# Optimization experiments

Measured on AMD Instinct MI355X. Metric: run time of the kernel, lower is better.

The kernel has to match this reference:

```python
import jax, jax.numpy as jnp
import numpy as np

B, N1, N2, C = 4, 1024, 128, 1152
H, D = 16, 72            # num_heads, head_dim (1152 = 16*72)
HID = 4608               # mlp hidden = 4*1152
ATTN_SCALE = D ** -0.5
RMS_SCALE = C ** 0.5     # quirk: RMSNorm built with dim=1152 though applied over d=72
LN_EPS = 1e-6


def setup_inputs() -> dict:
    key = jax.random.key(0)
    ks = iter(jax.random.split(key, 64))
    n = lambda shape, s=1.0: jax.random.normal(next(ks), shape, jnp.float32) * s
    W = 0.02  # weight init scale
    inp = {
        "x": n((B, N1, C)),
        "c": n((B, N2, C)),
        "global_c": n((B, C)),
        "ada_x_w": n((C, 6 * C), W), "ada_x_b": jnp.zeros((6 * C,)),
        "ada_c_w": n((C, 6 * C), W), "ada_c_b": jnp.zeros((6 * C,)),
        "g1x_g": jnp.ones((C,)), "g1x_b": jnp.zeros((C,)),
        "g2x_g": jnp.ones((C,)), "g2x_b": jnp.zeros((C,)),
        "g1c_g": jnp.ones((C,)), "g1c_b": jnp.zeros((C,)),
        "g2c_g": jnp.ones((C,)), "g2c_b": jnp.zeros((C,)),
        "qkv_x_w": n((C, 3 * C), W), "qkv_x_b": jnp.zeros((3 * C,)),
        "proj_x_w": n((C, C), W), "proj_x_b": jnp.zeros((C,)),
        "qkv_c_w": n((C, 3 * C), W), "qkv_c_b": jnp.zeros((3 * C,)),
        "proj_c_w": n((C, C), W), "proj_c_b": jnp.zeros((C,)),
        "gq_x": jnp.ones((1,)), "gk_x": jnp.ones((1,)),
        "gq_c": jnp.ones((1,)), "gk_c": jnp.ones((1,)),
        "mlp_x_w1": n((C, HID), W), "mlp_x_b1": jnp.zeros((HID,)),
        "mlp_x_w2": n((HID, C), W), "mlp_x_b2": jnp.zeros((C,)),
        "mlp_c_w1": n((C, HID), W), "mlp_c_b1": jnp.zeros((HID,)),
        "mlp_c_w2": n((HID, C), W), "mlp_c_b2": jnp.zeros((C,)),
    }
    return inp


def _ln(t, g, b):
    m = t.mean(-1, keepdims=True)
    v = ((t - m) ** 2).mean(-1, keepdims=True)
    return (t - m) * jax.lax.rsqrt(v + LN_EPS) * g + b


def _modulate(t, shift, scale):  # shift/scale: [B, C]
    return t * (1.0 + scale[:, None, :]) + shift[:, None, :]


def _rms(t, g):  # F.normalize over last dim, then * sqrt(1152) * g
    nrm = jnp.sqrt(jnp.sum(t * t, axis=-1, keepdims=True))
    return t / jnp.maximum(nrm, 1e-12) * (RMS_SCALE * g)


def _heads(t):  # [B, N, H*D] -> [B, H, N, D]
    Bq, Nq, _ = t.shape
    return t.reshape(Bq, Nq, H, D).transpose(0, 2, 1, 3)


def _mmdit_forward(x, c, global_c,
                   ada_x_w, ada_x_b, ada_c_w, ada_c_b,
                   g1x_g, g1x_b, g2x_g, g2x_b, g1c_g, g1c_b, g2c_g, g2c_b,
                   qkv_x_w, qkv_x_b, proj_x_w, proj_x_b,
                   qkv_c_w, qkv_c_b, proj_c_w, proj_c_b,
                   gq_x, gk_x, gq_c, gk_c,
                   mlp_x_w1, mlp_x_b1, mlp_x_w2, mlp_x_b2,
                   mlp_c_w1, mlp_c_b1, mlp_c_w2, mlp_c_b2):
    s = jax.nn.silu(global_c)
    mod_x = jnp.split(s @ ada_x_w + ada_x_b, 6, axis=-1)
    mod_c = jnp.split(s @ ada_c_w + ada_c_b, 6, axis=-1)
    (sh_msa_x, sc_msa_x, gt_msa_x, sh_mlp_x, sc_mlp_x, gt_mlp_x) = mod_x
    (sh_msa_c, sc_msa_c, gt_msa_c, sh_mlp_c, sc_mlp_c, gt_mlp_c) = mod_c

    xin = _modulate(_ln(x, g1x_g, g1x_b), sh_msa_x, sc_msa_x)
    cin = _modulate(_ln(c, g1c_g, g1c_b), sh_msa_c, sc_msa_c)

    qx, kx, vx = jnp.split(xin @ qkv_x_w + qkv_x_b, 3, axis=-1)
    qc, kc, vc = jnp.split(cin @ qkv_c_w + qkv_c_b, 3, axis=-1)
    qx, kx, vx = _heads(qx), _heads(kx), _heads(vx)
    qc, kc, vc = _heads(qc), _heads(kc), _heads(vc)
    qx, kx = _rms(qx, gq_x), _rms(kx, gk_x)
    qc, kc = _rms(qc, gq_c), _rms(kc, gk_c)

    q = jnp.concatenate([qx, qc], axis=2)  # [B,H,N1+N2,D]
    k = jnp.concatenate([kx, kc], axis=2)
    v = jnp.concatenate([vx, vc], axis=2)

    scores = jnp.einsum('bhnd,bhmd->bhnm', q, k) * ATTN_SCALE
    attn = jax.nn.softmax(scores, axis=-1)
    o = jnp.einsum('bhnm,bhmd->bhnd', attn, v)
    o = o.transpose(0, 2, 1, 3).reshape(B, N1 + N2, C)
    ox, oc = o[:, :N1], o[:, N1:]
    attn_x = ox @ proj_x_w + proj_x_b
    attn_c = oc @ proj_c_w + proj_c_b

    x = x + gt_msa_x[:, None, :] * attn_x
    c = c + gt_msa_c[:, None, :] * attn_c

    hx = _modulate(_ln(x, g2x_g, g2x_b), sh_mlp_x, sc_mlp_x)
    hx = jax.nn.gelu(hx @ mlp_x_w1 + mlp_x_b1, approximate=True) @ mlp_x_w2 + mlp_x_b2
    x = x + gt_mlp_x[:, None, :] * hx

    hc = _modulate(_ln(c, g2c_g, g2c_b), sh_mlp_c, sc_mlp_c)
    hc = jax.nn.gelu(hc @ mlp_c_w1 + mlp_c_b1, approximate=True) @ mlp_c_w2 + mlp_c_b2
    c = c + gt_mlp_c[:, None, :] * hc
    return x, c


def reference(x, c, global_c,
              ada_x_w, ada_x_b, ada_c_w, ada_c_b,
              g1x_g, g1x_b, g2x_g, g2x_b, g1c_g, g1c_b, g2c_g, g2c_b,
              qkv_x_w, qkv_x_b, proj_x_w, proj_x_b,
              qkv_c_w, qkv_c_b, proj_c_w, proj_c_b,
              gq_x, gk_x, gq_c, gk_c,
              mlp_x_w1, mlp_x_b1, mlp_x_w2, mlp_x_b2,
              mlp_c_w1, mlp_c_b1, mlp_c_w2, mlp_c_b2):
    return _mmdit_forward(x, c, global_c,
                          ada_x_w, ada_x_b, ada_c_w, ada_c_b,
                          g1x_g, g1x_b, g2x_g, g2x_b, g1c_g, g1c_b, g2c_g, g2c_b,
                          qkv_x_w, qkv_x_b, proj_x_w, proj_x_b,
                          qkv_c_w, qkv_c_b, proj_c_w, proj_c_b,
                          gq_x, gk_x, gq_c, gk_c,
                          mlp_x_w1, mlp_x_b1, mlp_x_w2, mlp_x_b2,
                          mlp_c_w1, mlp_c_b1, mlp_c_w2, mlp_c_b2)
```

## Files before the change

kernel.cpp:

```cpp
#include <hip/hip_runtime.h>

typedef unsigned short u16;
typedef unsigned int u32;
typedef __attribute__((ext_vector_type(8))) short bf16x8;
typedef __attribute__((ext_vector_type(4))) float f32x4;

#define MX_ 4096
#define NT_ 1152
#define C_  1152
#define DP_ 96
#define D_  72
#define H_  16

static __device__ __forceinline__ float b2f(u16 u){ union{u32 i; float f;} x; x.i=((u32)u)<<16; return x.f; }
static __device__ __forceinline__ u16 f2b(float f){ u32 i=__float_as_uint(f); return (u16)((i + 0x7FFFu + ((i>>16)&1u))>>16); }

static __device__ __forceinline__ void gl_lds16(const u16* g, u16* l){
  __builtin_amdgcn_global_load_lds((const __attribute__((address_space(1))) void*)g,
                                   (__attribute__((address_space(3))) void*)l, 16, 0, 0);
}

struct TrArgs {
  const float* src[8]; u16* dst[8]; int K[8]; int N[8]; int start[9];
};

__global__ __launch_bounds__(256) void transpose_kernel(TrArgs a){
  int bx = blockIdx.x;
  int mi = 0;
  #pragma unroll
  for (int i = 0; i < 8; ++i) if (bx >= a.start[i+1]) mi = i+1;
  int t = bx - a.start[mi];
  int K = a.K[mi], N = a.N[mi];
  int ntk = K >> 5;
  int tk = t % ntk, tn = t / ntk;
  int k0 = tk*32, n0 = tn*32;
  __shared__ u16 lds[32][33];
  int c = threadIdx.x & 31, r = threadIdx.x >> 5;
  const float* src = a.src[mi];
  u16* dst = a.dst[mi];
  #pragma unroll
  for (int ii = 0; ii < 4; ++ii){
    int row = r + ii*8;
    lds[row][c] = f2b(src[(size_t)(k0+row)*N + n0 + c]);
  }
  __syncthreads();
  #pragma unroll
  for (int ii = 0; ii < 4; ++ii){
    int row = r + ii*8;
    dst[(size_t)(n0+row)*K + k0 + c] = lds[c][row];
  }
}

__global__ __launch_bounds__(256) void ada_kernel(const float* gc, const float* wx, const float* bx,
                                                  const float* wc, const float* bc,
                                                  float* mod_x, float* mod_c){
  __shared__ float s[4][C_];
  __shared__ float part[4][4][64];
  int tid = threadIdx.x;
  for (int i = tid; i < 4*C_; i += 256){
    float v = gc[i];
    s[i / C_][i % C_] = v / (1.f + __expf(-v));
  }
  __syncthreads();
  int jq = tid & 63;
  int kq = tid >> 6;
  int jg = blockIdx.x*64 + jq;
  int which = jg / 6912;
  int j = jg % 6912;
  const float* W = which ? wc : wx;
  float a0=0.f, a1=0.f, a2=0.f, a3=0.f;
  for (int k = kq*288; k < kq*288 + 288; ++k){
    float w = W[(size_t)k*6912 + j];
    a0 += s[0][k]*w; a1 += s[1][k]*w; a2 += s[2][k]*w; a3 += s[3][k]*w;
  }
  part[kq][0][jq]=a0; part[kq][1][jq]=a1; part[kq][2][jq]=a2; part[kq][3][jq]=a3;
  __syncthreads();
  if (kq == 0){
    float bb = (which ? bc : bx)[j];
    float* out = which ? mod_c : mod_x;
    #pragma unroll
    for (int b = 0; b < 4; ++b){
      out[(size_t)b*6912 + j] = part[0][b][jq] + part[1][b][jq] + part[2][b][jq] + part[3][b][jq] + bb;
    }
  }
}

__global__ __launch_bounds__(256) void ln_mod_kernel(
  const float* srcx, const float* srcc, const float* g, const float* bt,
  const float* gcn, const float* btc,
  const float* shx, const float* scx, const float* shc, const float* scc,
  u16* out)
{
  int m = blockIdx.x;
  bool isC = (m >= MX_);
  const float* src = isC ? srcc + (size_t)(m - MX_)*C_ : srcx + (size_t)m*C_;
  int bidx = isC ? ((m - MX_) >> 7) : (m >> 10);
  const float* gg = isC ? gcn : g;
  const float* bb = isC ? btc : bt;
  const float* sh = (isC ? shc : shx) + (size_t)bidx*6912;
  const float* sc = (isC ? scc : scx) + (size_t)bidx*6912;
  int tid = threadIdx.x;
  float lv[8];
  float sum = 0.f, sq = 0.f;
  if (tid < 144){
    float4 v0 = *(const float4*)(src + tid*8);
    float4 v1 = *(const float4*)(src + tid*8 + 4);
    lv[0]=v0.x; lv[1]=v0.y; lv[2]=v0.z; lv[3]=v0.w;
    lv[4]=v1.x; lv[5]=v1.y; lv[6]=v1.z; lv[7]=v1.w;
    #pragma unroll
    for (int j = 0; j < 8; ++j){ sum += lv[j]; sq += lv[j]*lv[j]; }
  }
  #pragma unroll
  for (int off = 1; off < 64; off <<= 1){ sum += __shfl_xor(sum, off); sq += __shfl_xor(sq, off); }
  __shared__ float rs[4], rq[4];
  int wave = tid >> 6, lane = tid & 63;
  if (lane == 0){ rs[wave] = sum; rq[wave] = sq; }
  __syncthreads();
  float S = rs[0]+rs[1]+rs[2]+rs[3];
  float Q = rq[0]+rq[1]+rq[2]+rq[3];
  float mean = S * (1.f/1152.f);
  float var  = Q * (1.f/1152.f) - mean*mean;
  float rstd = rsqrtf(var + 1e-6f);
  if (tid < 144){
    union { uint4 v; u16 s[8]; } o;
    #pragma unroll
    for (int j = 0; j < 8; ++j){
      int n = tid*8 + j;
      float val = (lv[j] - mean)*rstd*gg[n] + bb[n];
      val = val*(1.f + sc[n]) + sh[n];
      o.s[j] = f2b(val);
    }
    *(uint4*)(out + (size_t)m*C_ + tid*8) = o.v;
  }
}

struct GemmArgs {
  const u16* A; int lda; int rowmap;
  const u16* BTx; const u16* BTc;
  const float* biasx; const float* biasc;
  void* outx; void* outc;
  const float* residx; const float* residc;
  const float* gatex; const float* gatec;
  int N, K;
};

static __device__ __forceinline__ int amap(int m, int rowmap){
  if (rowmap){
    if (m < MX_) return (m >> 10)*NT_ + (m & 1023);
    int mm = m - MX_;
    return (mm >> 7)*NT_ + 1024 + (mm & 127);
  }
  return m;
}

template<int EPI, int OF32>
__global__ __launch_bounds__(256, 2) void gemm_kernel(GemmArgs g){
  __shared__ u16 As[128*64];
  __shared__ u16 Bs[128*64];
  int n0 = blockIdx.x*128, m0 = blockIdx.y*128;
  bool isC = (m0 >= MX_);
  const u16* BT = isC ? g.BTc : g.BTx;
  int tid = threadIdx.x, wave = tid >> 6, lane = tid & 63;
  int lg = lane >> 4, lr = lane & 15;
  int wm = wave >> 1, wn = wave & 1;
  f32x4 acc[4][4] = {};
  for (int k0 = 0; k0 < g.K; k0 += 64){
    #pragma unroll
    for (int i = 0; i < 4; ++i){
      int cb = (wave*4 + i)*64;
      int q = cb + lane;
      int row = q >> 3;
      int c16 = (q & 7) ^ (row & 7);
      gl_lds16(g.A + (size_t)amap(m0 + row, g.rowmap)*g.lda + k0 + c16*8, As + cb*8);
      gl_lds16(BT + (size_t)(n0 + row)*g.K + k0 + c16*8, Bs + cb*8);
    }
    __syncthreads();
    #pragma unroll
    for (int kkI = 0; kkI < 2; ++kkI){
      bf16x8 af[4], bfr[4];
      #pragma unroll
      for (int mi = 0; mi < 4; ++mi){
        int row = wm*64 + mi*16 + lr;
        int c16 = (kkI*4 + lg) ^ (row & 7);
        af[mi] = *(const bf16x8*)&As[row*64 + c16*8];
      }
      #pragma unroll
      for (int ni = 0; ni < 4; ++ni){
        int row = wn*64 + ni*16 + lr;
        int c16 = (kkI*4 + lg) ^ (row & 7);
        bfr[ni] = *(const bf16x8*)&Bs[row*64 + c16*8];
      }
      #pragma unroll
      for (int mi = 0; mi < 4; ++mi)
        #pragma unroll
        for (int ni = 0; ni < 4; ++ni)
          acc[mi][ni] = __builtin_amdgcn_mfma_f32_16x16x32_bf16(af[mi], bfr[ni], acc[mi][ni], 0, 0, 0);
    }
    __syncthreads();
  }
  const float* bias  = isC ? g.biasc : g.biasx;
  const float* resid = isC ? g.residc : g.residx;
  void* out = isC ? g.outc : g.outx;
  const float* gate = nullptr;
  if (EPI == 2){
    int bidx = isC ? ((m0 - MX_) >> 7) : (m0 >> 10);
    gate = (isC ? g.gatec : g.gatex) + (size_t)bidx*6912;
  }
  int mbase = isC ? (m0 - MX_) : m0;
  #pragma unroll
  for (int mi = 0; mi < 4; ++mi){
    #pragma unroll
    for (int r = 0; r < 4; ++r){
      size_t orow = (size_t)(mbase + wm*64 + mi*16 + lg*4 + r);
      #pragma unroll
      for (int ni = 0; ni < 4; ++ni){
        int n = n0 + wn*64 + ni*16 + lr;
        float v = acc[mi][ni][r] + bias[n];
        if (EPI == 1){
          float u = 0.7978845608028654f*(v + 0.044715f*v*v*v);
          v = 0.5f*v*(1.f + tanhf(u));
        }
        if (EPI == 2){
          v = resid[orow*(size_t)g.N + n] + gate[n]*v;
        }
        if (OF32) ((float*)out)[orow*(size_t)g.N + n] = v;
        else      ((u16*)out)[orow*(size_t)g.N + n] = f2b(v);
      }
    }
  }
}

__global__ __launch_bounds__(256) void rmshead_kernel(
  const u16* qkv, const float* gqx, const float* gkx, const float* gqc, const float* gkc,
  u16* qpad, u16* kpad, u16* vT)
{
  int tt = blockIdx.x, h = blockIdx.y, b = blockIdx.z;
  int t0 = tt*64;
  bool isC = (t0 >= 1024);
  size_t rowbase = isC ? (size_t)(MX_ + b*128 + (t0 - 1024)) : (size_t)(b*1024 + t0);
  __shared__ u16 sq[2][64][72];
  __shared__ u16 sv[64][72];
  __shared__ float nf[2][64];
  int tid = threadIdx.x;
  for (int s = tid; s < 1728; s += 256){
    int which = s / 576, rem = s % 576;
    int t = rem / 9, ch = rem % 9;
    uint4 v = *(const uint4*)(qkv + (rowbase + t)*3456 + which*C_ + h*D_ + ch*8);
    u16* dst = (which < 2) ? &sq[which][t][ch*8] : &sv[t][ch*8];
    *(uint4*)dst = v;
  }
  __syncthreads();
  {
    int row = tid >> 1, half = tid & 1;
    int which = row >> 6, t = row & 63;
    float ss = 0.f;
    for (int d = half*36; d < half*36 + 36; ++d){
      float v = b2f(sq[which][t][d]); ss += v*v;
    }
    ss += __shfl_xor(ss, 1);
    if (half == 0){
      const float* gp = (which == 0) ? (isC ? gqc : gqx) : (isC ? gkc : gkx);
      nf[which][t] = 33.9411254970f * gp[0] / fmaxf(sqrtf(ss), 1e-12f);
    }
  }
  __syncthreads();
  size_t obase = ((size_t)(b*H_ + h)*NT_ + t0) * DP_;
  for (int s = tid; s < 1536; s += 256){
    int which = s / 768, rem = s % 768;
    int t = rem / 12, ch = rem % 12;
    float f = nf[which][t];
    union { uint4 v; u16 e[8]; } o;
    #pragma unroll
    for (int j = 0; j < 8; ++j){
      int d = ch*8 + j;
      o.e[j] = (d < D_) ? f2b(b2f(sq[which][t][d]) * f) : (u16)0;
    }
    *(uint4*)((which == 0 ? qpad : kpad) + obase + (size_t)t*DP_ + ch*8) = o.v;
  }
  size_t vbase = (size_t)(b*H_ + h)*80*NT_;
  for (int s = tid; s < 576; s += 256){
    int d = s / 8, ch = s % 8;
    union { uint4 v; u16 e[8]; } o;
    #pragma unroll
    for (int j = 0; j < 8; ++j) o.e[j] = sv[ch*8 + j][d];
    *(uint4*)(vT + vbase + (size_t)d*NT_ + t0 + ch*8) = o.v;
  }
}

__global__ __launch_bounds__(256, 2) void attn_kernel(
  const u16* qpad, const u16* kpad, const u16* vT, u16* O)
{
  int qt = blockIdx.x, h = blockIdx.y, b = blockIdx.z;
  int bh = b*H_ + h;
  __shared__ u16 Qs[64][104];
  __shared__ u16 Ks[64][104];
  __shared__ u16 Vs[80][72];
  __shared__ u16 Ps[64][72];
  __shared__ float fl[64];
  __shared__ float ll[64];
  int tid = threadIdx.x, wave = tid >> 6, lane = tid & 63;
  int lg = lane >> 4, lr = lane & 15;
  const u16* qbase = qpad + ((size_t)bh*NT_ + qt*64)*DP_;
  for (int i = wave; i < 13; i += 4){
    int slot = i*64 + lane;
    int row = slot / 13, ch = slot % 13;
    gl_lds16(qbase + (size_t)row*DP_ + ch*8, &Qs[0][0] + i*512);
  }
  f32x4 acc[5] = {};
  float m_r[4], l_r[4];
  #pragma unroll
  for (int r = 0; r < 4; ++r){ m_r[r] = -1e30f; l_r[r] = 0.f; }
  const u16* kbase0 = kpad + (size_t)bh*NT_*DP_;
  const u16* vbase0 = vT + (size_t)bh*80*NT_;
  for (int kvt = 0; kvt < 18; ++kvt){
    const u16* kb = kbase0 + (size_t)kvt*64*DP_;
    for (int i = wave; i < 13; i += 4){
      int slot = i*64 + lane;
      int row = slot / 13, ch = slot % 13;
      gl_lds16(kb + (size_t)row*DP_ + ch*8, &Ks[0][0] + i*512);
    }
    const u16* vb = vbase0 + kvt*64;
    for (int i = wave; i < 12; i += 4){
      int slot = i*64 + lane;
      if (slot < 720){
        int row = slot / 9, ch = slot % 9;
        gl_lds16(vb + (size_t)row*NT_ + ch*8, &Vs[0][0] + i*512);
      }
    }
    __syncthreads();
    f32x4 s[4] = {};
    bf16x8 aq[3];
    int qrow = wave*16 + lr;
    #pragma unroll
    for (int kkI = 0; kkI < 3; ++kkI) aq[kkI] = *(const bf16x8*)&Qs[qrow][(kkI*4 + lg)*8];
    #pragma unroll
    for (int nb = 0; nb < 4; ++nb){
      int krow = nb*16 + lr;
      #pragma unroll
      for (int kkI = 0; kkI < 3; ++kkI){
        bf16x8 bk = *(const bf16x8*)&Ks[krow][(kkI*4 + lg)*8];
        s[nb] = __builtin_amdgcn_mfma_f32_16x16x32_bf16(aq[kkI], bk, s[nb], 0, 0, 0);
      }
    }
    float p[4][4];
    #pragma unroll
    for (int nb = 0; nb < 4; ++nb)
      #pragma unroll
      for (int r = 0; r < 4; ++r) p[nb][r] = s[nb][r] * 0.11785113019775793f;
    float fac[4];
    #pragma unroll
    for (int r = 0; r < 4; ++r){
      float mx = fmaxf(fmaxf(p[0][r], p[1][r]), fmaxf(p[2][r], p[3][r]));
      #pragma unroll
      for (int off = 1; off < 16; off <<= 1) mx = fmaxf(mx, __shfl_xor(mx, off));
      float mn = fmaxf(m_r[r], mx);
      fac[r] = __expf(m_r[r] - mn);
      m_r[r] = mn;
      float rsum = 0.f;
      #pragma unroll
      for (int nb = 0; nb < 4; ++nb){ p[nb][r] = __expf(p[nb][r] - mn); rsum += p[nb][r]; }
      #pragma unroll
      for (int off = 1; off < 16; off <<= 1) rsum += __shfl_xor(rsum, off);
      l_r[r] = l_r[r]*fac[r] + rsum;
    }
    #pragma unroll
    for (int nb = 0; nb < 4; ++nb)
      #pragma unroll
      for (int r = 0; r < 4; ++r)
        Ps[wave*16 + lg*4 + r][nb*16 + lr] = f2b(p[nb][r]);
    if (lr == 0){
      #pragma unroll
      for (int r = 0; r < 4; ++r) fl[wave*16 + lg*4 + r] = fac[r];
    }
    __syncthreads();
    float fc = fl[wave*16 + lr];
    #pragma unroll
    for (int dc = 0; dc < 5; ++dc)
      #pragma unroll
      for (int j = 0; j < 4; ++j) acc[dc][j] *= fc;
    #pragma unroll
    for (int kkI = 0; kkI < 2; ++kkI){
      bf16x8 bp = *(const bf16x8*)&Ps[wave*16 + lr][(kkI*4 + lg)*8];
      #pragma unroll
      for (int dc = 0; dc < 5; ++dc){
        bf16x8 av = *(const bf16x8*)&Vs[dc*16 + lr][(kkI*4 + lg)*8];
        acc[dc] = __builtin_amdgcn_mfma_f32_16x16x32_bf16(av, bp, acc[dc], 0, 0, 0);
      }
    }
    __syncthreads();
  }
  if (lr == 0){
    #pragma unroll
    for (int r = 0; r < 4; ++r) ll[wave*16 + lg*4 + r] = l_r[r];
  }
  __syncthreads();
  float rl = 1.f / ll[wave*16 + lr];
  size_t orow = (size_t)b*NT_ + qt*64 + wave*16 + lr;
  #pragma unroll
  for (int dc = 0; dc < 5; ++dc){
    int d0 = dc*16 + lg*4;
    if (d0 < D_){
      union { uint2 v; u16 e[4]; } o;
      #pragma unroll
      for (int r = 0; r < 4; ++r) o.e[r] = f2b(acc[dc][r] * rl);
      *(uint2*)(O + orow*C_ + h*D_ + d0) = o.v;
    }
  }
}

extern "C" void kernel_launch(void* const* d_in, const int* in_sizes, int n_in,
                              void* d_out, int out_size, void* d_ws, size_t ws_size,
                              hipStream_t stream)
{
  (void)in_sizes; (void)n_in; (void)out_size; (void)ws_size;
  const float* x        = (const float*)d_in[0];
  const float* c        = (const float*)d_in[1];
  const float* gc       = (const float*)d_in[2];
  const float* ada_x_w  = (const float*)d_in[3];
  const float* ada_x_b  = (const float*)d_in[4];
  const float* ada_c_w  = (const float*)d_in[5];
  const float* ada_c_b  = (const float*)d_in[6];
  const float* g1x_g    = (const float*)d_in[7];
  const float* g1x_b    = (const float*)d_in[8];
  const float* g2x_g    = (const float*)d_in[9];
  const float* g2x_b    = (const float*)d_in[10];
  const float* g1c_g    = (const float*)d_in[11];
  const float* g1c_b    = (const float*)d_in[12];
  const float* g2c_g    = (const float*)d_in[13];
  const float* g2c_b    = (const float*)d_in[14];
  const float* qkv_x_w  = (const float*)d_in[15];
  const float* qkv_x_b  = (const float*)d_in[16];
  const float* proj_x_w = (const float*)d_in[17];
  const float* proj_x_b = (const float*)d_in[18];
  const float* qkv_c_w  = (const float*)d_in[19];
  const float* qkv_c_b  = (const float*)d_in[20];
  const float* proj_c_w = (const float*)d_in[21];
  const float* proj_c_b = (const float*)d_in[22];
  const float* gq_x     = (const float*)d_in[23];
  const float* gk_x     = (const float*)d_in[24];
  const float* gq_c     = (const float*)d_in[25];
  const float* gk_c     = (const float*)d_in[26];
  const float* m_x_w1   = (const float*)d_in[27];
  const float* m_x_b1   = (const float*)d_in[28];
  const float* m_x_w2   = (const float*)d_in[29];
  const float* m_x_b2   = (const float*)d_in[30];
  const float* m_c_w1   = (const float*)d_in[31];
  const float* m_c_b1   = (const float*)d_in[32];
  const float* m_c_w2   = (const float*)d_in[33];
  const float* m_c_b2   = (const float*)d_in[34];
  float* out = (float*)d_out;

  char* ws = (char*)d_ws;
  size_t off = 0;
  auto alloc = [&](size_t bytes)->void*{ void* p = ws + off; off += (bytes + 255) & ~(size_t)255; return p; };
  u16* WTqx  = (u16*)alloc((size_t)3456*1152*2);
  u16* WTqc  = (u16*)alloc((size_t)3456*1152*2);
  u16* WTpx  = (u16*)alloc((size_t)1152*1152*2);
  u16* WTpc  = (u16*)alloc((size_t)1152*1152*2);
  u16* WTm1x = (u16*)alloc((size_t)4608*1152*2);
  u16* WTm2x = (u16*)alloc((size_t)1152*4608*2);
  u16* WTm1c = (u16*)alloc((size_t)4608*1152*2);
  u16* WTm2c = (u16*)alloc((size_t)1152*4608*2);
  float* mod_x = (float*)alloc((size_t)4*6912*4);
  float* mod_c = (float*)alloc((size_t)4*6912*4);
  u16* xin  = (u16*)alloc((size_t)4608*1152*2);
  u16* pool = (u16*)alloc((size_t)4608*4608*2);
  u16* qpad = (u16*)alloc((size_t)64*1152*96*2 + 4096);
  u16* kpad = (u16*)alloc((size_t)64*1152*96*2 + 4096);
  u16* vTb  = (u16*)alloc((size_t)64*80*1152*2 + 4096);
  u16* Obuf = (u16*)alloc((size_t)4*1152*1152*2);
  float* x1c1 = (float*)alloc((size_t)4608*1152*4);

  {
    TrArgs ta;
    const float* srcs[8] = {qkv_x_w, qkv_c_w, proj_x_w, proj_c_w, m_x_w1, m_x_w2, m_c_w1, m_c_w2};
    u16* dsts[8]         = {WTqx, WTqc, WTpx, WTpc, WTm1x, WTm2x, WTm1c, WTm2c};
    int Ks[8] = {1152,1152,1152,1152,1152,4608,1152,4608};
    int Ns[8] = {3456,3456,1152,1152,4608,1152,4608,1152};
    int st = 0;
    for (int i = 0; i < 8; ++i){
      ta.src[i] = srcs[i]; ta.dst[i] = dsts[i]; ta.K[i] = Ks[i]; ta.N[i] = Ns[i];
      ta.start[i] = st; st += (Ks[i]/32)*(Ns[i]/32);
    }
    ta.start[8] = st;
    transpose_kernel<<<dim3(st), dim3(256), 0, stream>>>(ta);
  }
  ada_kernel<<<dim3(216), dim3(256), 0, stream>>>(gc, ada_x_w, ada_x_b, ada_c_w, ada_c_b, mod_x, mod_c);
  ln_mod_kernel<<<dim3(4608), dim3(256), 0, stream>>>(
      x, c, g1x_g, g1x_b, g1c_g, g1c_b,
      mod_x + 0, mod_x + 1152, mod_c + 0, mod_c + 1152, xin);
  {
    GemmArgs ga{};
    ga.A = xin; ga.lda = 1152; ga.rowmap = 0;
    ga.BTx = WTqx; ga.BTc = WTqc; ga.biasx = qkv_x_b; ga.biasc = qkv_c_b;
    ga.outx = pool; ga.outc = pool + (size_t)4096*3456;
    ga.N = 3456; ga.K = 1152;
    gemm_kernel<0,0><<<dim3(27,36), dim3(256), 0, stream>>>(ga);
  }
  rmshead_kernel<<<dim3(18,16,4), dim3(256), 0, stream>>>(pool, gq_x, gk_x, gq_c, gk_c, qpad, kpad, vTb);
  attn_kernel<<<dim3(18,16,4), dim3(256), 0, stream>>>(qpad, kpad, vTb, Obuf);
  {
    GemmArgs ga{};
    ga.A = Obuf; ga.lda = 1152; ga.rowmap = 1;
    ga.BTx = WTpx; ga.BTc = WTpc; ga.biasx = proj_x_b; ga.biasc = proj_c_b;
    ga.outx = x1c1; ga.outc = x1c1 + (size_t)4096*1152;
    ga.residx = x; ga.residc = c;
    ga.gatex = mod_x + 2*1152; ga.gatec = mod_c + 2*1152;
    ga.N = 1152; ga.K = 1152;
    gemm_kernel<2,1><<<dim3(9,36), dim3(256), 0, stream>>>(ga);
  }
  ln_mod_kernel<<<dim3(4608), dim3(256), 0, stream>>>(
      x1c1, x1c1 + (size_t)4096*1152, g2x_g, g2x_b, g2c_g, g2c_b,
      mod_x + 3*1152, mod_x + 4*1152, mod_c + 3*1152, mod_c + 4*1152, xin);
  {
    GemmArgs ga{};
    ga.A = xin; ga.lda = 1152; ga.rowmap = 0;
    ga.BTx = WTm1x; ga.BTc = WTm1c; ga.biasx = m_x_b1; ga.biasc = m_c_b1;
    ga.outx = pool; ga.outc = pool + (size_t)4096*4608;
    ga.N = 4608; ga.K = 1152;
    gemm_kernel<1,0><<<dim3(36,36), dim3(256), 0, stream>>>(ga);
  }
  {
    GemmArgs ga{};
    ga.A = pool; ga.lda = 4608; ga.rowmap = 0;
    ga.BTx = WTm2x; ga.BTc = WTm2c; ga.biasx = m_x_b2; ga.biasc = m_c_b2;
    ga.outx = out; ga.outc = out + (size_t)4096*1152;
    ga.residx = x1c1; ga.residc = x1c1 + (size_t)4096*1152;
    ga.gatex = mod_x + 5*1152; ga.gatec = mod_c + 5*1152;
    ga.N = 1152; ga.K = 4608;
    gemm_kernel<2,1><<<dim3(9,36), dim3(256), 0, stream>>>(ga);
  }
}
```

Baseline: 488.3 us.

## Double-buffer GEMM LDS tiles and load attention K/V directly into registers

The GEMM kernel now double-buffers its A/B LDS tiles and precomputes per-thread global addresses, so the next K-slice streams in while the current one is multiplied. The attention kernel drops its Q/K/V LDS staging and most block barriers. Each wave loads its Q, K and V fragments straight from global memory into registers, and MFMA sections run at raised wave priority. The QKV prep kernel now zero-fills the padded V rows 72-79, because the attention kernel reads them from global memory. This trades LDS traffic and syncs for redundant global/L2 loads across waves, and doubles GEMM LDS use, which may hurt occupancy.

```diff
diff --git a/kernel.cpp b/kernel.cpp
--- a/kernel.cpp
+++ b/kernel.cpp
@@ -155,8 +155,8 @@
 
 template<int EPI, int OF32>
 __global__ __launch_bounds__(256, 2) void gemm_kernel(GemmArgs g){
-  __shared__ u16 As[128*64];
-  __shared__ u16 Bs[128*64];
+  __shared__ u16 As[2][128*64];
+  __shared__ u16 Bs[2][128*64];
   int n0 = blockIdx.x*128, m0 = blockIdx.y*128;
   bool isC = (m0 >= MX_);
   const u16* BT = isC ? g.BTc : g.BTx;
@@ -164,17 +164,26 @@
   int lg = lane >> 4, lr = lane & 15;
   int wm = wave >> 1, wn = wave & 1;
   f32x4 acc[4][4] = {};
-  for (int k0 = 0; k0 < g.K; k0 += 64){
+
+  const u16* Aaddr[4]; const u16* Baddr[4];
+  #pragma unroll
+  for (int i = 0; i < 4; ++i){
+    int cb = (wave*4 + i)*64;
+    int q = cb + lane;
+    int row = q >> 3;
+    int c16 = (q & 7) ^ (row & 7);
+    Aaddr[i] = g.A + (size_t)amap(m0 + row, g.rowmap)*g.lda + c16*8;
+    Baddr[i] = BT + (size_t)(n0 + row)*g.K + c16*8;
+  }
+  auto STAGE = [&](int buf, int k0){
     #pragma unroll
     for (int i = 0; i < 4; ++i){
       int cb = (wave*4 + i)*64;
-      int q = cb + lane;
-      int row = q >> 3;
-      int c16 = (q & 7) ^ (row & 7);
-      gl_lds16(g.A + (size_t)amap(m0 + row, g.rowmap)*g.lda + k0 + c16*8, As + cb*8);
-      gl_lds16(BT + (size_t)(n0 + row)*g.K + k0 + c16*8, Bs + cb*8);
-    }
-    __syncthreads();
+      gl_lds16(Aaddr[i] + k0, &As[buf][cb*8]);
+      gl_lds16(Baddr[i] + k0, &Bs[buf][cb*8]);
+    }
+  };
+  auto COMPUTE = [&](int buf){
     #pragma unroll
     for (int kkI = 0; kkI < 2; ++kkI){
       bf16x8 af[4], bfr[4];
@@ -182,13 +191,13 @@
       for (int mi = 0; mi < 4; ++mi){
         int row = wm*64 + mi*16 + lr;
         int c16 = (kkI*4 + lg) ^ (row & 7);
-        af[mi] = *(const bf16x8*)&As[row*64 + c16*8];
+        af[mi] = *(const bf16x8*)&As[buf][row*64 + c16*8];
       }
       #pragma unroll
       for (int ni = 0; ni < 4; ++ni){
         int row = wn*64 + ni*16 + lr;
         int c16 = (kkI*4 + lg) ^ (row & 7);
-        bfr[ni] = *(const bf16x8*)&Bs[row*64 + c16*8];
+        bfr[ni] = *(const bf16x8*)&Bs[buf][row*64 + c16*8];
       }
       #pragma unroll
       for (int mi = 0; mi < 4; ++mi)
@@ -196,8 +205,22 @@
         for (int ni = 0; ni < 4; ++ni)
           acc[mi][ni] = __builtin_amdgcn_mfma_f32_16x16x32_bf16(af[mi], bfr[ni], acc[mi][ni], 0, 0, 0);
     }
+  };
+
+  int nk = g.K >> 6;
+  STAGE(0, 0);
+  asm volatile("s_waitcnt vmcnt(0)" ::: "memory");
+  __syncthreads();
+  int cur = 0;
+  for (int t = 0; t < nk - 1; ++t){
+    STAGE(cur ^ 1, (t+1)*64);
+    COMPUTE(cur);
+    asm volatile("s_waitcnt vmcnt(0)" ::: "memory");
     __syncthreads();
-  }
+    cur ^= 1;
+  }
+  COMPUTE(cur);
+
   const float* bias  = isC ? g.biasc : g.biasx;
   const float* resid = isC ? g.residc : g.residx;
   void* out = isC ? g.outc : g.outx;
@@ -285,63 +308,53 @@
     for (int j = 0; j < 8; ++j) o.e[j] = sv[ch*8 + j][d];
     *(uint4*)(vT + vbase + (size_t)d*NT_ + t0 + ch*8) = o.v;
   }
-}
-
-__global__ __launch_bounds__(256, 2) void attn_kernel(
+  for (int s = tid; s < 512; s += 256){
+    int d = 72 + (s >> 6), t = s & 63;
+    vT[vbase + (size_t)d*NT_ + t0 + t] = 0;
+  }
+}
+
+#define PS_ 76
+__global__ __launch_bounds__(256) void attn_kernel(
   const u16* qpad, const u16* kpad, const u16* vT, u16* O)
 {
   int qt = blockIdx.x, h = blockIdx.y, b = blockIdx.z;
   int bh = b*H_ + h;
-  __shared__ u16 Qs[64][104];
-  __shared__ u16 Ks[64][104];
-  __shared__ u16 Vs[80][72];
-  __shared__ u16 Ps[64][72];
+  __shared__ u16 Ps[64][PS_];
   __shared__ float fl[64];
   __shared__ float ll[64];
   int tid = threadIdx.x, wave = tid >> 6, lane = tid & 63;
   int lg = lane >> 4, lr = lane & 15;
-  const u16* qbase = qpad + ((size_t)bh*NT_ + qt*64)*DP_;
-  for (int i = wave; i < 13; i += 4){
-    int slot = i*64 + lane;
-    int row = slot / 13, ch = slot % 13;
-    gl_lds16(qbase + (size_t)row*DP_ + ch*8, &Qs[0][0] + i*512);
-  }
+
+  const u16* qbase = qpad + ((size_t)bh*NT_ + qt*64 + wave*16 + lr)*DP_;
+  bf16x8 aq[3];
+  #pragma unroll
+  for (int kkI = 0; kkI < 3; ++kkI) aq[kkI] = *(const bf16x8*)(qbase + (kkI*4 + lg)*8);
+
   f32x4 acc[5] = {};
   float m_r[4], l_r[4];
   #pragma unroll
   for (int r = 0; r < 4; ++r){ m_r[r] = -1e30f; l_r[r] = 0.f; }
-  const u16* kbase0 = kpad + (size_t)bh*NT_*DP_;
-  const u16* vbase0 = vT + (size_t)bh*80*NT_;
+  const u16* kb0 = kpad + (size_t)bh*NT_*DP_;
+  const u16* vb0 = vT + (size_t)bh*80*NT_;
+
   for (int kvt = 0; kvt < 18; ++kvt){
-    const u16* kb = kbase0 + (size_t)kvt*64*DP_;
-    for (int i = wave; i < 13; i += 4){
-      int slot = i*64 + lane;
-      int row = slot / 13, ch = slot % 13;
-      gl_lds16(kb + (size_t)row*DP_ + ch*8, &Ks[0][0] + i*512);
-    }
-    const u16* vb = vbase0 + kvt*64;
-    for (int i = wave; i < 12; i += 4){
-      int slot = i*64 + lane;
-      if (slot < 720){
-        int row = slot / 9, ch = slot % 9;
-        gl_lds16(vb + (size_t)row*NT_ + ch*8, &Vs[0][0] + i*512);
-      }
-    }
-    __syncthreads();
+    const u16* kb = kb0 + (size_t)kvt*64*DP_;
+    bf16x8 bk[4][3];
+    #pragma unroll
+    for (int nb = 0; nb < 4; ++nb)
+      #pragma unroll
+      for (int kkI = 0; kkI < 3; ++kkI)
+        bk[nb][kkI] = *(const bf16x8*)(kb + (size_t)(nb*16 + lr)*DP_ + (kkI*4 + lg)*8);
     f32x4 s[4] = {};
-    bf16x8 aq[3];
-    int qrow = wave*16 + lr;
-    #pragma unroll
-    for (int kkI = 0; kkI < 3; ++kkI) aq[kkI] = *(const bf16x8*)&Qs[qrow][(kkI*4 + lg)*8];
-    #pragma unroll
-    for (int nb = 0; nb < 4; ++nb){
-      int krow = nb*16 + lr;
-      #pragma unroll
-      for (int kkI = 0; kkI < 3; ++kkI){
-        bf16x8 bk = *(const bf16x8*)&Ks[krow][(kkI*4 + lg)*8];
-        s[nb] = __builtin_amdgcn_mfma_f32_16x16x32_bf16(aq[kkI], bk, s[nb], 0, 0, 0);
-      }
-    }
+    __builtin_amdgcn_s_setprio(1);
+    #pragma unroll
+    for (int nb = 0; nb < 4; ++nb)
+      #pragma unroll
+      for (int kkI = 0; kkI < 3; ++kkI)
+        s[nb] = __builtin_amdgcn_mfma_f32_16x16x32_bf16(aq[kkI], bk[nb][kkI], s[nb], 0, 0, 0);
+    __builtin_amdgcn_s_setprio(0);
+
     float p[4][4];
     #pragma unroll
     for (int nb = 0; nb < 4; ++nb)
@@ -372,28 +385,27 @@
       #pragma unroll
       for (int r = 0; r < 4; ++r) fl[wave*16 + lg*4 + r] = fac[r];
     }
-    __syncthreads();
     float fc = fl[wave*16 + lr];
     #pragma unroll
     for (int dc = 0; dc < 5; ++dc)
       #pragma unroll
       for (int j = 0; j < 4; ++j) acc[dc][j] *= fc;
+    __builtin_amdgcn_s_setprio(1);
     #pragma unroll
     for (int kkI = 0; kkI < 2; ++kkI){
       bf16x8 bp = *(const bf16x8*)&Ps[wave*16 + lr][(kkI*4 + lg)*8];
       #pragma unroll
       for (int dc = 0; dc < 5; ++dc){
-        bf16x8 av = *(const bf16x8*)&Vs[dc*16 + lr][(kkI*4 + lg)*8];
+        bf16x8 av = *(const bf16x8*)(vb0 + (size_t)(dc*16 + lr)*NT_ + kvt*64 + (kkI*4 + lg)*8);
         acc[dc] = __builtin_amdgcn_mfma_f32_16x16x32_bf16(av, bp, acc[dc], 0, 0, 0);
       }
     }
-    __syncthreads();
+    __builtin_amdgcn_s_setprio(0);
   }
   if (lr == 0){
     #pragma unroll
     for (int r = 0; r < 4; ++r) ll[wave*16 + lg*4 + r] = l_r[r];
   }
-  __syncthreads();
   float rl = 1.f / ll[wave*16 + lr];
   size_t orow = (size_t)b*NT_ + qt*64 + wave*16 + lr;
   #pragma unroll
```

Measured after the change: 590.5 us. 20.9% more time.
